# Optimization experiments

Hardware: AMD Instinct MI355X
Metric: run time of the kernel (lower is better)

Reference implementation:

```python
import jax, jax.numpy as jnp
import numpy as np

N_NODES = 50000
N_EDGES = 800000
IN_F = 256
OUT_F = 128
ALPHA = 0.2  # LeakyReLU negative slope


def setup_inputs() -> dict:
    key = jax.random.key(0)
    k_h, k_row, k_col, k_W, k_a = jax.random.split(key, 5)
    h = jax.random.normal(k_h, (N_NODES, IN_F), dtype=jnp.float32)
    row = jax.random.randint(k_row, (N_EDGES,), 0, N_NODES)
    # Guarantee every node appears as a destination so unique(dst) == arange(N)
    col = jnp.concatenate([
        jnp.arange(N_NODES),
        jax.random.randint(k_col, (N_EDGES - N_NODES,), 0, N_NODES),
    ])
    adj = jnp.stack([row, col]).astype(jnp.int64)
    # Xavier-uniform-ish params (gain 1.414)
    lim_W = 1.414 * np.sqrt(6.0 / (IN_F + OUT_F))
    W = jax.random.uniform(k_W, (IN_F, OUT_F), minval=-lim_W, maxval=lim_W, dtype=jnp.float32)
    lim_a = 1.414 * np.sqrt(6.0 / (2 * OUT_F + 1))
    a = jax.random.uniform(k_a, (2 * OUT_F, 1), minval=-lim_a, maxval=lim_a, dtype=jnp.float32)
    return {"h": h, "adj": adj, "W": W, "a": a}


def reference(h, adj, W, a):
    N = h.shape[0]
    self_loops = jnp.arange(N)  # == unique(adj[1]) by input construction
    row = jnp.concatenate([adj[0], self_loops])  # [E_total]
    col = jnp.concatenate([adj[1], self_loops])  # [E_total]

    Wh = h @ W                                    # [N, OUT_F]
    s_src = (Wh @ a[:OUT_F]).squeeze(-1)          # [N] (Wh1)
    s_dst = (Wh @ a[OUT_F:]).squeeze(-1)          # [N] (Wh2)

    e = jax.nn.leaky_relu(s_dst[col] + s_src[row], negative_slope=ALPHA)  # [E_total]

    # segment softmax over destination nodes
    e_max = jax.ops.segment_max(e, col, num_segments=N)
    ex = jnp.exp(e - e_max[col])
    denom = jax.ops.segment_sum(ex, col, num_segments=N)
    att = ex / denom[col]                         # [E_total]

    h_prime = jax.ops.segment_sum(Wh[row] * att[:, None], col, num_segments=N)  # [N, OUT_F]
    return jax.nn.elu(h_prime)  # concat=True
```

## Files before the change

### kernel.cpp

```cpp
#include <hip/hip_runtime.h>
#include <math.h>

#define N_NODES 50000
#define N_EDGES 800000
#define IN_F 256
#define OUT_F 128
#define ALPHA 0.2f

#define B_DST 32
#define B_EDGE 16
#define R_NODES 1563
#define CHUNK_E (N_EDGES / B_EDGE)
#define CAP_C 12
#define RAW_STRIDE (B_EDGE * CAP_C)
#define SCAT_BLOCKS (B_DST * B_EDGE)
#define SLOT_CAP 64

#define CONV_BLOCKS (N_NODES * IN_F / 8 / 256)
#define COMPACT_BLOCKS ((N_NODES + 255) / 256)
#define GEMM_WAVES ((N_NODES + 15) / 16)
#define GEMM_BLOCKS ((GEMM_WAVES + 3) / 4)

typedef short bf16x8 __attribute__((ext_vector_type(8)));
typedef float f32x4  __attribute__((ext_vector_type(4)));

static __device__ __forceinline__ unsigned short f2bf(float f) {
    unsigned int u = __float_as_uint(f);
    u += 0x7FFFu + ((u >> 16) & 1u);
    return (unsigned short)(u >> 16);
}
static __device__ __forceinline__ float bf2f(unsigned int u16) {
    return __uint_as_float(u16 << 16);
}

__global__ __launch_bounds__(256, 4) void k_scat(const int* __restrict__ adj,
                                                 unsigned short* __restrict__ slots_raw,
                                                 unsigned char* __restrict__ cnt8) {
    const int b = blockIdx.x, t = threadIdx.x;
    const int j  = b % B_EDGE;
    const int di = b / B_EDGE;
    const int base = di * R_NODES;
    const int lim  = min(base + R_NODES, N_NODES);
    __shared__ int cl[R_NODES];
    for (int k = t; k < R_NODES; k += 256) cl[k] = 0;
    __syncthreads();
    const int e0 = j * CHUNK_E;
    const int4* dp = (const int4*)(adj + N_EDGES + e0);
    const int4* sp = (const int4*)(adj + e0);
    const int nit = CHUNK_E / 4;
    for (int it0 = t; it0 < nit; it0 += 1024) {
        int4 dv[4], sv[4];
#pragma unroll
        for (int u = 0; u < 4; ++u) {
            const int it = it0 + u * 256;
            if (it < nit) { dv[u] = dp[it]; sv[u] = sp[it]; }
            else          { dv[u] = make_int4(-1, -1, -1, -1); sv[u] = make_int4(0, 0, 0, 0); }
        }
#pragma unroll
        for (int u = 0; u < 4; ++u) {
            const int4 d = dv[u], s = sv[u];
            if (d.x >= base && d.x < lim) {
                const int p = atomicAdd(&cl[d.x - base], 1);
                if (p < CAP_C) slots_raw[(size_t)d.x * RAW_STRIDE + j * CAP_C + p] = (unsigned short)s.x;
            }
            if (d.y >= base && d.y < lim) {
                const int p = atomicAdd(&cl[d.y - base], 1);
                if (p < CAP_C) slots_raw[(size_t)d.y * RAW_STRIDE + j * CAP_C + p] = (unsigned short)s.y;
            }
            if (d.z >= base && d.z < lim) {
                const int p = atomicAdd(&cl[d.z - base], 1);
                if (p < CAP_C) slots_raw[(size_t)d.z * RAW_STRIDE + j * CAP_C + p] = (unsigned short)s.z;
            }
            if (d.w >= base && d.w < lim) {
                const int p = atomicAdd(&cl[d.w - base], 1);
                if (p < CAP_C) slots_raw[(size_t)d.w * RAW_STRIDE + j * CAP_C + p] = (unsigned short)s.w;
            }
        }
    }
    __syncthreads();
    for (int k = t; k < lim - base; k += 256)
        cnt8[(size_t)(base + k) * B_EDGE + j] = (unsigned char)min(cl[k], CAP_C);
}

__global__ __launch_bounds__(256) void k_prep2(const float* __restrict__ W,
                                               const float* __restrict__ h,
                                               unsigned short* __restrict__ WbT,
                                               unsigned short* __restrict__ hb) {
    const int b = blockIdx.x, t = threadIdx.x;
    if (b < OUT_F) {
        WbT[(size_t)b * IN_F + t] = f2bf(W[(size_t)t * OUT_F + b]);
        return;
    }
    const size_t base = ((size_t)(b - OUT_F) * 256 + t) * 8;
    const float4* hp = (const float4*)(h + base);
    const float4 x0 = hp[0], x1 = hp[1];
    bf16x8 v;
    v[0] = (short)f2bf(x0.x); v[1] = (short)f2bf(x0.y);
    v[2] = (short)f2bf(x0.z); v[3] = (short)f2bf(x0.w);
    v[4] = (short)f2bf(x1.x); v[5] = (short)f2bf(x1.y);
    v[6] = (short)f2bf(x1.z); v[7] = (short)f2bf(x1.w);
    *(bf16x8*)(hb + base) = v;
}

__global__ __launch_bounds__(256, 4) void k_gemm(const unsigned short* __restrict__ hb,
                                                 const unsigned short* __restrict__ WbT,
                                                 const float* __restrict__ a,
                                                 unsigned short* __restrict__ Whb,
                                                 float* __restrict__ s_src,
                                                 float* __restrict__ s_dst,
                                                 unsigned short* __restrict__ slots_raw,
                                                 const unsigned char* __restrict__ cnt8,
                                                 int* __restrict__ cntT) {
    const int b = blockIdx.x;
    if (b < COMPACT_BLOCKS) {
        const int node = b * 256 + threadIdx.x;
        if (node >= N_NODES) return;
        const unsigned char* c8 = cnt8 + (size_t)node * B_EDGE;
        unsigned short* row = slots_raw + (size_t)node * RAW_STRIDE;
        int total = 0;
#pragma unroll
        for (int c = 0; c < B_EDGE; ++c) {
            const int dc = c8[c];
            const unsigned short* s = row + c * CAP_C;
            for (int k = 0; k < dc; ++k) {
                const unsigned short v = s[k];
                if (total < SLOT_CAP) row[total++] = v;
            }
        }
        cntT[node] = total;
        return;
    }
    const int gid = b - COMPACT_BLOCKS;
    const int wid = gid * 4 + (threadIdx.x >> 6);
    if (wid >= GEMM_WAVES) return;
    const int lane = threadIdx.x & 63;
    const int m = lane & 15, grp = lane >> 4;
    const int row = wid * 16 + m;
    const unsigned short* hrow = hb + (size_t)row * IN_F + grp * 8;
    const unsigned short* wbase = WbT + (size_t)m * IN_F + grp * 8;

    bf16x8 hf[8];
#pragma unroll
    for (int kt = 0; kt < 8; ++kt) hf[kt] = *(const bf16x8*)(hrow + kt * 32);

    f32x4 acc[8];
#pragma unroll
    for (int nt = 0; nt < 8; ++nt) acc[nt] = (f32x4){0.f, 0.f, 0.f, 0.f};
#pragma unroll
    for (int kt = 0; kt < 8; ++kt) {
#pragma unroll
        for (int nt = 0; nt < 8; ++nt) {
            bf16x8 wf = *(const bf16x8*)(wbase + (size_t)nt * 16 * IN_F + kt * 32);
            acc[nt] = __builtin_amdgcn_mfma_f32_16x16x32_bf16(wf, hf[kt], acc[nt], 0, 0, 0);
        }
    }

    float s1 = 0.0f, s2 = 0.0f;
#pragma unroll
    for (int nt = 0; nt < 8; ++nt) {
        const float4 a1 = *(const float4*)(a + nt * 16 + grp * 4);
        const float4 a2 = *(const float4*)(a + OUT_F + nt * 16 + grp * 4);
        const f32x4 v = acc[nt];
        s1 = fmaf(v[0], a1.x, fmaf(v[1], a1.y, fmaf(v[2], a1.z, fmaf(v[3], a1.w, s1))));
        s2 = fmaf(v[0], a2.x, fmaf(v[1], a2.y, fmaf(v[2], a2.z, fmaf(v[3], a2.w, s2))));
    }
    s1 += __shfl_xor(s1, 16); s1 += __shfl_xor(s1, 32);
    s2 += __shfl_xor(s2, 16); s2 += __shfl_xor(s2, 32);
    if (grp == 0) { s_src[row] = s1; s_dst[row] = s2; }

    unsigned short* orow = Whb + (size_t)row * OUT_F;
#pragma unroll
    for (int nt = 0; nt < 8; ++nt) {
        f32x4 v = acc[nt];
        ushort4 pk;
        pk.x = f2bf(v[0]); pk.y = f2bf(v[1]);
        pk.z = f2bf(v[2]); pk.w = f2bf(v[3]);
        *(ushort4*)(orow + nt * 16 + grp * 4) = pk;
    }
}

__global__ __launch_bounds__(256, 4) void k_gather(const unsigned short* __restrict__ Whb,
                                                   const int* __restrict__ cntT,
                                                   const unsigned short* __restrict__ slots_raw,
                                                   const float* __restrict__ s_src,
                                                   const float* __restrict__ s_dst,
                                                   float* __restrict__ out) {
    const int wid  = (blockIdx.x * blockDim.x + threadIdx.x) >> 6;
    const int lane = threadIdx.x & 63;
    const int grp  = lane >> 4;
    const int l    = lane & 15;
    const int node = wid * 4 + grp;
    if (node >= N_NODES) return;

    const float sd = s_dst[node];
    float s0 = sd + s_src[node];
    float lr0 = (s0 > 0.0f) ? s0 : ALPHA * s0;
    float x0 = __expf(lr0);
    uint4 w0 = ((const uint4*)(Whb + (size_t)node * OUT_F))[l];
    float a0 = x0 * bf2f(w0.x & 0xFFFFu);
    float a1 = x0 * bf2f(w0.x >> 16);
    float a2 = x0 * bf2f(w0.y & 0xFFFFu);
    float a3 = x0 * bf2f(w0.y >> 16);
    float a4 = x0 * bf2f(w0.z & 0xFFFFu);
    float a5 = x0 * bf2f(w0.z >> 16);
    float a6 = x0 * bf2f(w0.w & 0xFFFFu);
    float a7 = x0 * bf2f(w0.w >> 16);
    float dsum = x0;

    const int deg = min(cntT[node], SLOT_CAP);
    const unsigned short* __restrict__ srow = slots_raw + (size_t)node * RAW_STRIDE;

    for (int i = 0; i < deg; i += 8) {
        const uint4 q = *(const uint4*)(srow + i);
        unsigned su[8];
        su[0] = q.x & 0xFFFFu; su[1] = q.x >> 16;
        su[2] = q.y & 0xFFFFu; su[3] = q.y >> 16;
        su[4] = q.z & 0xFFFFu; su[5] = q.z >> 16;
        su[6] = q.w & 0xFFFFu; su[7] = q.w >> 16;
#pragma unroll
        for (int j = 0; j < 8; ++j)
            su[j] = (i + j < deg) ? min(su[j], N_NODES - 1u) : (unsigned)node;
        float e[8];
#pragma unroll
        for (int j = 0; j < 8; ++j) e[j] = sd + s_src[su[j]];
        uint4 v[8];
#pragma unroll
        for (int j = 0; j < 8; ++j) v[j] = ((const uint4*)(Whb + (size_t)su[j] * OUT_F))[l];
        float x[8];
#pragma unroll
        for (int j = 0; j < 8; ++j) {
            float lr = (e[j] > 0.0f) ? e[j] : ALPHA * e[j];
            float xv = __expf(lr);
            x[j] = (i + j < deg) ? xv : 0.0f;
        }
#pragma unroll
        for (int j = 0; j < 8; ++j) dsum += x[j];
#pragma unroll
        for (int j = 0; j < 8; ++j) {
            a0 = fmaf(x[j], bf2f(v[j].x & 0xFFFFu), a0);
            a1 = fmaf(x[j], bf2f(v[j].x >> 16), a1);
            a2 = fmaf(x[j], bf2f(v[j].y & 0xFFFFu), a2);
            a3 = fmaf(x[j], bf2f(v[j].y >> 16), a3);
            a4 = fmaf(x[j], bf2f(v[j].z & 0xFFFFu), a4);
            a5 = fmaf(x[j], bf2f(v[j].z >> 16), a5);
            a6 = fmaf(x[j], bf2f(v[j].w & 0xFFFFu), a6);
            a7 = fmaf(x[j], bf2f(v[j].w >> 16), a7);
        }
    }

    const float inv = 1.0f / dsum;
    float4 o0, o1;
    o0.x = a0 * inv; o0.y = a1 * inv; o0.z = a2 * inv; o0.w = a3 * inv;
    o1.x = a4 * inv; o1.y = a5 * inv; o1.z = a6 * inv; o1.w = a7 * inv;
    o0.x = (o0.x > 0.0f) ? o0.x : expm1f(o0.x);
    o0.y = (o0.y > 0.0f) ? o0.y : expm1f(o0.y);
    o0.z = (o0.z > 0.0f) ? o0.z : expm1f(o0.z);
    o0.w = (o0.w > 0.0f) ? o0.w : expm1f(o0.w);
    o1.x = (o1.x > 0.0f) ? o1.x : expm1f(o1.x);
    o1.y = (o1.y > 0.0f) ? o1.y : expm1f(o1.y);
    o1.z = (o1.z > 0.0f) ? o1.z : expm1f(o1.z);
    o1.w = (o1.w > 0.0f) ? o1.w : expm1f(o1.w);
    float4* op = (float4*)(out + (size_t)node * OUT_F + l * 8);
    op[0] = o0;
    op[1] = o1;
}

extern "C" void kernel_launch(void* const* d_in, const int* in_sizes, int n_in,
                              void* d_out, int out_size, void* d_ws, size_t ws_size,
                              hipStream_t stream) {
    const float* h   = (const float*)d_in[0];
    const int*   adj = (const int*)d_in[1];
    const float* W   = (const float*)d_in[2];
    const float* a   = (const float*)d_in[3];
    float* out = (float*)d_out;

    char* ws = (char*)d_ws;
    const size_t SZ_WHB  = (size_t)N_NODES * OUT_F * 2;
    const size_t SZ_N    = 200704;
    const size_t SZ_C8   = 802816;
    const size_t SZ_RAW  = (size_t)N_NODES * RAW_STRIDE * 2;
    unsigned short* Whb   = (unsigned short*)(ws);
    float* s_src          = (float*)(ws + SZ_WHB);
    float* s_dst          = (float*)(ws + SZ_WHB + SZ_N);
    int*   cntT           = (int*)  (ws + SZ_WHB + 2 * SZ_N);
    unsigned short* WbT   = (unsigned short*)(ws + SZ_WHB + 3 * SZ_N);
    unsigned char* cnt8   = (unsigned char*)(ws + SZ_WHB + 3 * SZ_N + 65536);
    unsigned short* slots_raw = (unsigned short*)(ws + SZ_WHB + 3 * SZ_N + 65536 + SZ_C8);
    unsigned short* hb    = (unsigned short*)(ws + SZ_WHB + 3 * SZ_N + 65536 + SZ_C8 + SZ_RAW);

    (void)in_sizes; (void)n_in; (void)out_size; (void)ws_size;

    k_scat  <<<SCAT_BLOCKS, 256, 0, stream>>>(adj, slots_raw, cnt8);
    k_prep2 <<<OUT_F + CONV_BLOCKS, 256, 0, stream>>>(W, h, WbT, hb);
    k_gemm  <<<COMPACT_BLOCKS + GEMM_BLOCKS, 256, 0, stream>>>(hb, WbT, a, Whb,
                                                               s_src, s_dst,
                                                               slots_raw, cnt8, cntT);
    k_gather<<<(N_NODES / 4 * 64) / 256, 256, 0, stream>>>(Whb, cntT, slots_raw,
                                                           s_src, s_dst, out);
}
```

Baseline: 208.4 us.

## Stage W in swizzled LDS for GEMM and widen edge scatter partitioning

The GEMM kernel now cooperatively loads the full bf16 transposed W (64 KB) into LDS with an XOR swizzle, so each wave reads its W fragments from shared memory rather than global/L2. Rows are clamped and stores guarded so the final partial block stays safe, and the occupancy hint drops to 2 blocks per SM to fit the LDS. Separately, the edge scatter uses 32 edge chunks with per-chunk capacity 10 instead of 16 chunks with capacity 12, and the cnt8 buffer size now follows B_EDGE. The larger LDS footprint limits occupancy, and the smaller per-chunk capacity raises the risk of dropping edges.

```diff
diff --git a/kernel.cpp b/kernel.cpp
--- a/kernel.cpp
+++ b/kernel.cpp
@@ -8,18 +8,18 @@
 #define ALPHA 0.2f
 
 #define B_DST 32
-#define B_EDGE 16
+#define B_EDGE 32
 #define R_NODES 1563
 #define CHUNK_E (N_EDGES / B_EDGE)
-#define CAP_C 12
+#define CAP_C 10
 #define RAW_STRIDE (B_EDGE * CAP_C)
 #define SCAT_BLOCKS (B_DST * B_EDGE)
 #define SLOT_CAP 64
 
 #define CONV_BLOCKS (N_NODES * IN_F / 8 / 256)
 #define COMPACT_BLOCKS ((N_NODES + 255) / 256)
-#define GEMM_WAVES ((N_NODES + 15) / 16)
-#define GEMM_BLOCKS ((GEMM_WAVES + 3) / 4)
+#define GEMM_BLOCKS ((N_NODES + 63) / 64)
+#define GEMM_WAVES_TOT (GEMM_BLOCKS * 4)
 
 typedef short bf16x8 __attribute__((ext_vector_type(8)));
 typedef float f32x4  __attribute__((ext_vector_type(4)));
@@ -102,7 +102,7 @@
     *(bf16x8*)(hb + base) = v;
 }
 
-__global__ __launch_bounds__(256, 4) void k_gemm(const unsigned short* __restrict__ hb,
+__global__ __launch_bounds__(256, 2) void k_gemm(const unsigned short* __restrict__ hb,
                                                  const unsigned short* __restrict__ WbT,
                                                  const float* __restrict__ a,
                                                  unsigned short* __restrict__ Whb,
@@ -130,14 +130,22 @@
         cntT[node] = total;
         return;
     }
+    __shared__ unsigned short wlds[32768];
+    const int t = threadIdx.x;
+    for (int s = t; s < 4096; s += 256) {
+        const int col = s >> 5, k8 = s & 31;
+        const bf16x8 v = *(const bf16x8*)(WbT + (size_t)col * IN_F + k8 * 8);
+        *(bf16x8*)(wlds + ((size_t)col * 32 + (k8 ^ (col & 7))) * 8) = v;
+    }
+    __syncthreads();
+
     const int gid = b - COMPACT_BLOCKS;
-    const int wid = gid * 4 + (threadIdx.x >> 6);
-    if (wid >= GEMM_WAVES) return;
-    const int lane = threadIdx.x & 63;
+    const int w = t >> 6;
+    const int lane = t & 63;
     const int m = lane & 15, grp = lane >> 4;
-    const int row = wid * 16 + m;
-    const unsigned short* hrow = hb + (size_t)row * IN_F + grp * 8;
-    const unsigned short* wbase = WbT + (size_t)m * IN_F + grp * 8;
+    const int row = gid * 64 + w * 16 + m;
+    const int rowc = min(row, N_NODES - 1);
+    const unsigned short* hrow = hb + (size_t)rowc * IN_F + grp * 8;
 
     bf16x8 hf[8];
 #pragma unroll
@@ -150,7 +158,9 @@
     for (int kt = 0; kt < 8; ++kt) {
 #pragma unroll
         for (int nt = 0; nt < 8; ++nt) {
-            bf16x8 wf = *(const bf16x8*)(wbase + (size_t)nt * 16 * IN_F + kt * 32);
+            const int col = nt * 16 + m;
+            const int k8 = kt * 4 + grp;
+            const bf16x8 wf = *(const bf16x8*)(wlds + ((size_t)col * 32 + (k8 ^ (col & 7))) * 8);
             acc[nt] = __builtin_amdgcn_mfma_f32_16x16x32_bf16(wf, hf[kt], acc[nt], 0, 0, 0);
         }
     }
@@ -166,16 +176,17 @@
     }
     s1 += __shfl_xor(s1, 16); s1 += __shfl_xor(s1, 32);
     s2 += __shfl_xor(s2, 16); s2 += __shfl_xor(s2, 32);
-    if (grp == 0) { s_src[row] = s1; s_dst[row] = s2; }
-
-    unsigned short* orow = Whb + (size_t)row * OUT_F;
-#pragma unroll
-    for (int nt = 0; nt < 8; ++nt) {
-        f32x4 v = acc[nt];
-        ushort4 pk;
-        pk.x = f2bf(v[0]); pk.y = f2bf(v[1]);
-        pk.z = f2bf(v[2]); pk.w = f2bf(v[3]);
-        *(ushort4*)(orow + nt * 16 + grp * 4) = pk;
+    if (row < N_NODES) {
+        if (grp == 0) { s_src[row] = s1; s_dst[row] = s2; }
+        unsigned short* orow = Whb + (size_t)row * OUT_F;
+#pragma unroll
+        for (int nt = 0; nt < 8; ++nt) {
+            f32x4 v = acc[nt];
+            ushort4 pk;
+            pk.x = f2bf(v[0]); pk.y = f2bf(v[1]);
+            pk.z = f2bf(v[2]); pk.w = f2bf(v[3]);
+            *(ushort4*)(orow + nt * 16 + grp * 4) = pk;
+        }
     }
 }
 
@@ -277,7 +288,7 @@
     char* ws = (char*)d_ws;
     const size_t SZ_WHB  = (size_t)N_NODES * OUT_F * 2;
     const size_t SZ_N    = 200704;
-    const size_t SZ_C8   = 802816;
+    const size_t SZ_C8   = (size_t)N_NODES * B_EDGE;
     const size_t SZ_RAW  = (size_t)N_NODES * RAW_STRIDE * 2;
     unsigned short* Whb   = (unsigned short*)(ws);
     float* s_src          = (float*)(ws + SZ_WHB);
```

Measured after the change: 201.3 us. 3.4% less time.

## Fuse edge scatter and bf16 conversion into one interleaved front kernel

Applied to the files above, without the earlier changes.

Merges the edge-bucketing scatter kernel and the W/h bf16 conversion kernel into a single launch, interleaving one scatter block every seven block indices so latency-bound atomic scatter work overlaps with bandwidth-bound conversion work. It also doubles the number of edge chunks per destination range and lowers the per-chunk slot capacity, which changes the raw slot and count buffer sizes. This removes one kernel launch boundary and lets the two phases share the GPU. Risks include more LDS pressure for the conversion blocks (the shared array is now in the fused kernel), a different overflow behaviour with the smaller per-chunk cap, and downstream kernels that must agree with the new B_EDGE layout.

```diff
diff --git a/kernel.cpp b/kernel.cpp
--- a/kernel.cpp
+++ b/kernel.cpp
@@ -8,15 +8,17 @@
 #define ALPHA 0.2f
 
 #define B_DST 32
-#define B_EDGE 16
+#define B_EDGE 32
 #define R_NODES 1563
 #define CHUNK_E (N_EDGES / B_EDGE)
-#define CAP_C 12
+#define CAP_C 10
 #define RAW_STRIDE (B_EDGE * CAP_C)
 #define SCAT_BLOCKS (B_DST * B_EDGE)
 #define SLOT_CAP 64
 
 #define CONV_BLOCKS (N_NODES * IN_F / 8 / 256)
+#define STREAM_BLOCKS (OUT_F + CONV_BLOCKS)
+#define FRONT_BLOCKS (SCAT_BLOCKS + STREAM_BLOCKS)
 #define COMPACT_BLOCKS ((N_NODES + 255) / 256)
 #define GEMM_WAVES ((N_NODES + 15) / 16)
 #define GEMM_BLOCKS ((GEMM_WAVES + 3) / 4)
@@ -33,65 +35,70 @@
     return __uint_as_float(u16 << 16);
 }
 
-__global__ __launch_bounds__(256, 4) void k_scat(const int* __restrict__ adj,
-                                                 unsigned short* __restrict__ slots_raw,
-                                                 unsigned char* __restrict__ cnt8) {
+__global__ __launch_bounds__(256, 4) void k_front(const float* __restrict__ W,
+                                                  const float* __restrict__ h,
+                                                  const int* __restrict__ adj,
+                                                  unsigned short* __restrict__ WbT,
+                                                  unsigned short* __restrict__ hb,
+                                                  unsigned short* __restrict__ slots_raw,
+                                                  unsigned char* __restrict__ cnt8) {
     const int b = blockIdx.x, t = threadIdx.x;
-    const int j  = b % B_EDGE;
-    const int di = b / B_EDGE;
-    const int base = di * R_NODES;
-    const int lim  = min(base + R_NODES, N_NODES);
-    __shared__ int cl[R_NODES];
-    for (int k = t; k < R_NODES; k += 256) cl[k] = 0;
-    __syncthreads();
-    const int e0 = j * CHUNK_E;
-    const int4* dp = (const int4*)(adj + N_EDGES + e0);
-    const int4* sp = (const int4*)(adj + e0);
-    const int nit = CHUNK_E / 4;
-    for (int it0 = t; it0 < nit; it0 += 1024) {
-        int4 dv[4], sv[4];
-#pragma unroll
-        for (int u = 0; u < 4; ++u) {
-            const int it = it0 + u * 256;
-            if (it < nit) { dv[u] = dp[it]; sv[u] = sp[it]; }
-            else          { dv[u] = make_int4(-1, -1, -1, -1); sv[u] = make_int4(0, 0, 0, 0); }
-        }
-#pragma unroll
-        for (int u = 0; u < 4; ++u) {
-            const int4 d = dv[u], s = sv[u];
-            if (d.x >= base && d.x < lim) {
-                const int p = atomicAdd(&cl[d.x - base], 1);
-                if (p < CAP_C) slots_raw[(size_t)d.x * RAW_STRIDE + j * CAP_C + p] = (unsigned short)s.x;
+    const bool is_scat = ((b % 7) == 3) && (b / 7 < SCAT_BLOCKS);
+    if (is_scat) {
+        const int sb = b / 7;
+        const int j  = sb % B_EDGE;
+        const int di = sb / B_EDGE;
+        const int base = di * R_NODES;
+        const int lim  = min(base + R_NODES, N_NODES);
+        __shared__ int cl[R_NODES];
+        for (int k = t; k < R_NODES; k += 256) cl[k] = 0;
+        __syncthreads();
+        const int e0 = j * CHUNK_E;
+        const int4* dp = (const int4*)(adj + N_EDGES + e0);
+        const int4* sp = (const int4*)(adj + e0);
+        const int nit = CHUNK_E / 4;
+        for (int it0 = t; it0 < nit; it0 += 1024) {
+            int4 dv[4], sv[4];
+#pragma unroll
+            for (int u = 0; u < 4; ++u) {
+                const int it = it0 + u * 256;
+                if (it < nit) { dv[u] = dp[it]; sv[u] = sp[it]; }
+                else          { dv[u] = make_int4(-1, -1, -1, -1); sv[u] = make_int4(0, 0, 0, 0); }
             }
-            if (d.y >= base && d.y < lim) {
-                const int p = atomicAdd(&cl[d.y - base], 1);
-                if (p < CAP_C) slots_raw[(size_t)d.y * RAW_STRIDE + j * CAP_C + p] = (unsigned short)s.y;
+#pragma unroll
+            for (int u = 0; u < 4; ++u) {
+                const int4 d = dv[u], s = sv[u];
+                if (d.x >= base && d.x < lim) {
+                    const int p = atomicAdd(&cl[d.x - base], 1);
+                    if (p < CAP_C) slots_raw[(size_t)d.x * RAW_STRIDE + j * CAP_C + p] = (unsigned short)s.x;
+                }
+                if (d.y >= base && d.y < lim) {
+                    const int p = atomicAdd(&cl[d.y - base], 1);
+                    if (p < CAP_C) slots_raw[(size_t)d.y * RAW_STRIDE + j * CAP_C + p] = (unsigned short)s.y;
+                }
+                if (d.z >= base && d.z < lim) {
+                    const int p = atomicAdd(&cl[d.z - base], 1);
+                    if (p < CAP_C) slots_raw[(size_t)d.z * RAW_STRIDE + j * CAP_C + p] = (unsigned short)s.z;
+                }
+                if (d.w >= base && d.w < lim) {
+                    const int p = atomicAdd(&cl[d.w - base], 1);
+                    if (p < CAP_C) slots_raw[(size_t)d.w * RAW_STRIDE + j * CAP_C + p] = (unsigned short)s.w;
+                }
             }
-            if (d.z >= base && d.z < lim) {
-                const int p = atomicAdd(&cl[d.z - base], 1);
-                if (p < CAP_C) slots_raw[(size_t)d.z * RAW_STRIDE + j * CAP_C + p] = (unsigned short)s.z;
-            }
-            if (d.w >= base && d.w < lim) {
-                const int p = atomicAdd(&cl[d.w - base], 1);
-                if (p < CAP_C) slots_raw[(size_t)d.w * RAW_STRIDE + j * CAP_C + p] = (unsigned short)s.w;
-            }
-        }
-    }
-    __syncthreads();
-    for (int k = t; k < lim - base; k += 256)
-        cnt8[(size_t)(base + k) * B_EDGE + j] = (unsigned char)min(cl[k], CAP_C);
-}
-
-__global__ __launch_bounds__(256) void k_prep2(const float* __restrict__ W,
-                                               const float* __restrict__ h,
-                                               unsigned short* __restrict__ WbT,
-                                               unsigned short* __restrict__ hb) {
-    const int b = blockIdx.x, t = threadIdx.x;
-    if (b < OUT_F) {
-        WbT[(size_t)b * IN_F + t] = f2bf(W[(size_t)t * OUT_F + b]);
+        }
+        __syncthreads();
+        for (int k = t; k < lim - base; k += 256)
+            cnt8[(size_t)(base + k) * B_EDGE + j] = (unsigned char)min(cl[k], CAP_C);
         return;
     }
-    const size_t base = ((size_t)(b - OUT_F) * 256 + t) * 8;
+    int ns = b / 7 + (((b % 7) > 3) ? 1 : 0);
+    if (ns > SCAT_BLOCKS) ns = SCAT_BLOCKS;
+    const int sid = b - ns;
+    if (sid < OUT_F) {
+        WbT[(size_t)sid * IN_F + t] = f2bf(W[(size_t)t * OUT_F + sid]);
+        return;
+    }
+    const size_t base = ((size_t)(sid - OUT_F) * 256 + t) * 8;
     const float4* hp = (const float4*)(h + base);
     const float4 x0 = hp[0], x1 = hp[1];
     bf16x8 v;
@@ -277,7 +284,7 @@
     char* ws = (char*)d_ws;
     const size_t SZ_WHB  = (size_t)N_NODES * OUT_F * 2;
     const size_t SZ_N    = 200704;
-    const size_t SZ_C8   = 802816;
+    const size_t SZ_C8   = (size_t)N_NODES * B_EDGE;
     const size_t SZ_RAW  = (size_t)N_NODES * RAW_STRIDE * 2;
     unsigned short* Whb   = (unsigned short*)(ws);
     float* s_src          = (float*)(ws + SZ_WHB);
@@ -290,8 +297,7 @@
 
     (void)in_sizes; (void)n_in; (void)out_size; (void)ws_size;
 
-    k_scat  <<<SCAT_BLOCKS, 256, 0, stream>>>(adj, slots_raw, cnt8);
-    k_prep2 <<<OUT_F + CONV_BLOCKS, 256, 0, stream>>>(W, h, WbT, hb);
+    k_front <<<FRONT_BLOCKS, 256, 0, stream>>>(W, h, adj, WbT, hb, slots_raw, cnt8);
     k_gemm  <<<COMPACT_BLOCKS + GEMM_BLOCKS, 256, 0, stream>>>(hb, WbT, a, Whb,
                                                                s_src, s_dst,
                                                                slots_raw, cnt8, cntT);
```

Measured after the change: 232.2 us. 1.11x slower.
